# Performance work log

Hardware: AMD Instinct MI355X
Metric: run time of the kernel (lower is better)

Reference implementation:

```python
import jax, jax.numpy as jnp
import numpy as np

B, N, FEAT, MSG, LINK_H, CLS = 8, 128, 1024, 256, 512, 600
PROP = 2  # propagate_layers


def setup_inputs() -> dict:
    key = jax.random.key(0)
    ks = jax.random.split(key, 16)
    g = lambda k, shape, s=0.02: jax.random.normal(k, shape, dtype=jnp.float32) * s
    inp = {
        'edge_features': g(ks[0], (B, N, N, FEAT), 1.0),
        'node_features': g(ks[1], (B, N, FEAT), 1.0),
        'adj_mat': jnp.zeros((B, N, N), jnp.float32),          # shape placeholder only
        'node_labels': jnp.zeros((B, N, CLS), jnp.float32),    # shape placeholder only
        'human_nums': 64,
        'obj_nums': 64,
        # feature resize linears (Linear(FEAT -> MSG))
        'W_er': g(ks[2], (MSG, FEAT)), 'b_er': jnp.zeros((MSG,), jnp.float32),
        'W_nr': g(ks[3], (MSG, FEAT)), 'b_nr': jnp.zeros((MSG,), jnp.float32),
        # link fun (GraphConv): 1x1 Conv2d(MSG->LINK_H), ReLU, 1x1 Conv2d(LINK_H->1)
        'W_l1': g(ks[4], (LINK_H, MSG)), 'b_l1': jnp.zeros((LINK_H,), jnp.float32),
        'W_l2': g(ks[5], (1, LINK_H)), 'b_l2': jnp.zeros((1,), jnp.float32),
        # message fun linear_concat_relu: Linear(node+edge = 2*MSG -> MSG), ReLU
        'W_m': g(ks[6], (MSG, 2 * MSG)), 'b_m': jnp.zeros((MSG,), jnp.float32),
        # GRU(input=MSG, hidden=MSG), single layer single step
        'W_ih': g(ks[7], (3 * MSG, MSG)), 'b_ih': jnp.zeros((3 * MSG,), jnp.float32),
        'W_hh': g(ks[8], (3 * MSG, MSG)), 'b_hh': jnp.zeros((3 * MSG,), jnp.float32),
        # readout fc: Linear(MSG -> CLS)
        'W_r': g(ks[9], (CLS, MSG)), 'b_r': jnp.zeros((CLS,), jnp.float32),
    }
    return inp


def reference(edge_features, node_features, adj_mat, node_labels,
              human_nums, obj_nums,
              W_er, b_er, W_nr, b_nr, W_l1, b_l1, W_l2, b_l2,
              W_m, b_m, W_ih, b_ih, W_hh, b_hh, W_r, b_r):
    # valid_node_num = human_nums + obj_nums == N for every batch element.
    # Resize raw features to message size.
    e = edge_features @ W_er.T + b_er        # [B, v, w, MSG]
    h = node_features @ W_nr.T + b_nr        # [B, w, MSG]  (node states are never rewritten in source)
    # Split concat-linear into two matmuls to avoid materializing [B,N,N,2*MSG].
    W_mh, W_me = W_m[:, :MSG], W_m[:, MSG:]
    msg_h = jnp.einsum('bwd,md->bwm', h, W_mh)                 # node part, shared over target v
    msg_e = jnp.einsum('bvwd,md->bvwm', e, W_me) + b_m          # edge part (original e, constant over rounds)
    edge_state = e
    m = None
    pred_adj = None
    for _ in range(PROP):
        # link fun: per-(v,w) MLP over channels (1x1 convs)
        x = jax.nn.relu(edge_state @ W_l1.T + b_l1)             # [B,v,w,LINK_H]
        pred_adj = (x @ W_l2.T + b_l2)[..., 0]                  # [B,N,N]
        sig = jax.nn.sigmoid(pred_adj)
        # message fun linear_concat_relu, gated by predicted adjacency
        m = jax.nn.relu(msg_h[:, None, :, :] + msg_e)           # [B,v,w,MSG]
        m = sig[..., None] * m
        # hidden_edge_states[round+1][:, :, w, v] = m_v[:, :, w]
        edge_state = jnp.swapaxes(m, 1, 2)
    # node update happens per node each round but hidden node states are never
    # written back in the source, so only the last round's GRU step matters.
    m_sum = m.sum(axis=2)                                       # [B,v,MSG]
    gi = m_sum @ W_ih.T + b_ih
    gh = h @ W_hh.T + b_hh
    ir, iz, inn = jnp.split(gi, 3, axis=-1)
    hr, hz, hn = jnp.split(gh, 3, axis=-1)
    r = jax.nn.sigmoid(ir + hr)
    z = jax.nn.sigmoid(iz + hz)
    n = jnp.tanh(inn + r * hn)
    h_new = (1.0 - z) * n + z * h                               # [B,N,MSG]
    pred_node_labels = h_new @ W_r.T + b_r                      # [B,N,CLS]
    return pred_adj, pred_node_labels
```

## Files before the change

### kernel.cpp

```cpp
#include <hip/hip_runtime.h>
#include <cstdint>
#include <cstddef>

#define NND   128
#define FEATD 1024
#define MSGD  256
#define LHD   512
#define CLSD  600
#define LDST  264

typedef __bf16 bf16_t;
typedef bf16_t bf16x8 __attribute__((ext_vector_type(8)));
typedef float  f32x4  __attribute__((ext_vector_type(4)));
typedef unsigned short u16;
typedef u16 u16x8 __attribute__((ext_vector_type(8)));
typedef u16 u16x4 __attribute__((ext_vector_type(4)));

static __device__ __forceinline__ float bf2f(u16 u) {
  union { unsigned u; float f; } x; x.u = ((unsigned)u) << 16; return x.f;
}
static __device__ __forceinline__ u16 f2bf(float f) {
  union { float f; unsigned u; } x; x.f = f;
  return (u16)((x.u + 0x7fffu + ((x.u >> 16) & 1u)) >> 16);
}
static __device__ __forceinline__ f32x4 mfma16(u16x8 a, u16x8 b, f32x4 c) {
  return __builtin_amdgcn_mfma_f32_16x16x32_bf16(
      __builtin_bit_cast(bf16x8, a), __builtin_bit_cast(bf16x8, b), c, 0, 0, 0);
}
static __device__ __forceinline__ f32x4 zero4() {
  f32x4 v; v[0] = 0.f; v[1] = 0.f; v[2] = 0.f; v[3] = 0.f; return v;
}
static __device__ __forceinline__ float sigm(float x) { return 1.0f / (1.0f + expf(-x)); }

__global__ void k_cvt(const float* __restrict__ src, u16* __restrict__ dst, int n) {
  int i = (blockIdx.x * 256 + threadIdx.x) * 4;
  if (i + 3 < n) {
    float4 f = *(const float4*)(src + i);
    u16x4 o; o[0] = f2bf(f.x); o[1] = f2bf(f.y); o[2] = f2bf(f.z); o[3] = f2bf(f.w);
    *(u16x4*)(dst + i) = o;
  }
}

__global__ __launch_bounds__(256) void k_comb(const float* __restrict__ Wm,
                                              const float* __restrict__ Wer,
                                              const float* __restrict__ b_er,
                                              const float* __restrict__ b_m,
                                              u16* __restrict__ WcombB,
                                              float* __restrict__ bcomb) {
  const int m = blockIdx.x >> 2, ch = blockIdx.x & 3;
  const int d = ch * 256 + threadIdx.x;
  float s = 0.f;
  for (int k = 0; k < 256; ++k)
    s += Wm[(size_t)m * 512 + 256 + k] * Wer[(size_t)k * FEATD + d];
  WcombB[(size_t)m * FEATD + d] = f2bf(s);
  if (ch == 0 && threadIdx.x == 0) {
    float bb2 = b_m[m];
    for (int k = 0; k < 256; ++k) bb2 += Wm[(size_t)m * 512 + 256 + k] * b_er[k];
    bcomb[m] = bb2;
  }
}

__global__ __launch_bounds__(256) void s1_hmsg(const float* __restrict__ node,
                                               const float* __restrict__ Wnr,
                                               const float* __restrict__ bnr,
                                               const float* __restrict__ Wm,
                                               float* __restrict__ h32,
                                               u16* __restrict__ msghB) {
  __shared__ float nrow[FEATD];
  __shared__ float hrow[MSGD];
  const int r = blockIdx.x;
  const int t = threadIdx.x;
  *(float4*)(&nrow[t * 4]) = *(const float4*)(node + (size_t)r * FEATD + t * 4);
  __syncthreads();
  float acc = bnr[t];
  for (int d = 0; d < FEATD; ++d) acc += nrow[d] * Wnr[(size_t)t * FEATD + d];
  h32[(size_t)r * MSGD + t] = acc;
  hrow[t] = acc;
  __syncthreads();
  float mh = 0.f;
  for (int k = 0; k < MSGD; ++k) mh += hrow[k] * Wm[(size_t)t * 2 * MSGD + k];
  msghB[(size_t)r * MSGD + t] = f2bf(mh);
}

__global__ __launch_bounds__(512, 4) void k_main(
    const float* __restrict__ edge, const u16* __restrict__ Wer, const u16* __restrict__ Wm,
    const u16* __restrict__ Wl1, const float* __restrict__ b_er, const float* __restrict__ b_m,
    const float* __restrict__ b_l1, const float* __restrict__ W_l2, const float* __restrict__ b_l2,
    const u16* __restrict__ msgh, u16* __restrict__ M0g, float* __restrict__ pa_out) {
  __shared__ __align__(16) u16 lsE[64][LDST];
  __shared__ __align__(16) u16 lsM[64][LDST];
  __shared__ float lsPA[8][64];
  __shared__ float lsSig[64];

  const int tid = threadIdx.x, lane = tid & 63, wave = tid >> 6;
  const int lh = lane & 15, lq = lane >> 4;
  const int base = blockIdx.x * 64;
  const int bb = base >> 14;
  const int vv = (base >> 7) & 127;
  const int w0 = base & 127;

  f32x4 acc[4][4];

#pragma unroll
  for (int m = 0; m < 4; ++m)
#pragma unroll
    for (int t = 0; t < 2; ++t) acc[m][t] = zero4();
  for (int kc = 0; kc < 4; ++kc) {
#pragma unroll
    for (int i = 0; i < 8; ++i) {
      int idx = tid + i * 512;
      int row = idx >> 6;
      int c4 = (idx & 63) << 2;
      float4 f = *(const float4*)(edge + (size_t)(base + row) * FEATD + kc * 256 + c4);
      u16x4 o; o[0] = f2bf(f.x); o[1] = f2bf(f.y); o[2] = f2bf(f.z); o[3] = f2bf(f.w);
      *(u16x4*)(&lsE[row][c4]) = o;
    }
    __syncthreads();
#pragma unroll
    for (int ks = 0; ks < 8; ++ks) {
      u16x8 afr[4];
#pragma unroll
      for (int m = 0; m < 4; ++m) afr[m] = *(const u16x8*)(&lsE[16 * m + lh][ks * 32 + lq * 8]);
      const int kg = kc * 256 + ks * 32 + lq * 8;
#pragma unroll
      for (int t = 0; t < 2; ++t) {
        int col = wave * 32 + t * 16 + lh;
        u16x8 bfr = *(const u16x8*)(Wer + (size_t)col * FEATD + kg);
#pragma unroll
        for (int m = 0; m < 4; ++m) acc[m][t] = mfma16(afr[m], bfr, acc[m][t]);
      }
    }
    __syncthreads();
  }
#pragma unroll
  for (int t = 0; t < 2; ++t) {
    int col = wave * 32 + t * 16 + lh;
    float be = b_er[col];
#pragma unroll
    for (int m = 0; m < 4; ++m)
#pragma unroll
      for (int j = 0; j < 4; ++j)
        lsE[16 * m + 4 * lq + j][col] = f2bf(acc[m][t][j] + be);
  }
  __syncthreads();

  float prow[4][4];
#pragma unroll
  for (int m = 0; m < 4; ++m)
#pragma unroll
    for (int j = 0; j < 4; ++j) prow[m][j] = 0.f;
#pragma unroll
  for (int m = 0; m < 4; ++m)
#pragma unroll
    for (int t = 0; t < 4; ++t) acc[m][t] = zero4();
#pragma unroll
  for (int ks = 0; ks < 8; ++ks) {
    u16x8 afr[4];
#pragma unroll
    for (int m = 0; m < 4; ++m) afr[m] = *(const u16x8*)(&lsE[16 * m + lh][ks * 32 + lq * 8]);
    const int kg = ks * 32 + lq * 8;
#pragma unroll
    for (int t = 0; t < 4; ++t) {
      int col = wave * 64 + t * 16 + lh;
      u16x8 bfr = *(const u16x8*)(Wl1 + (size_t)col * MSGD + kg);
#pragma unroll
      for (int m = 0; m < 4; ++m) acc[m][t] = mfma16(afr[m], bfr, acc[m][t]);
    }
  }
#pragma unroll
  for (int t = 0; t < 4; ++t) {
    int col = wave * 64 + t * 16 + lh;
    float bl = b_l1[col], wl = W_l2[col];
#pragma unroll
    for (int m = 0; m < 4; ++m)
#pragma unroll
      for (int j = 0; j < 4; ++j) prow[m][j] += fmaxf(acc[m][t][j] + bl, 0.f) * wl;
  }
#pragma unroll
  for (int off = 1; off < 16; off <<= 1)
#pragma unroll
    for (int m = 0; m < 4; ++m)
#pragma unroll
      for (int j = 0; j < 4; ++j) prow[m][j] += __shfl_xor(prow[m][j], off, 64);
  if (lh == 0) {
#pragma unroll
    for (int m = 0; m < 4; ++m)
#pragma unroll
      for (int j = 0; j < 4; ++j) lsPA[wave][16 * m + 4 * lq + j] = prow[m][j];
  }
  __syncthreads();
  if (tid < 64) {
    float pa1 = b_l2[0];
#pragma unroll
    for (int g = 0; g < 8; ++g) pa1 += lsPA[g][tid];
    lsSig[tid] = sigm(pa1);
  }
#pragma unroll
  for (int i = 0; i < 4; ++i) {
    int idx = tid + i * 512;
    int row = idx >> 5;
    int c8 = (idx & 31) << 3;
    *(u16x8*)(&lsM[row][c8]) =
        *(const u16x8*)(msgh + (size_t)(bb * NND + w0 + row) * MSGD + c8);
  }
  __syncthreads();

#pragma unroll
  for (int m = 0; m < 4; ++m)
#pragma unroll
    for (int t = 0; t < 2; ++t) acc[m][t] = zero4();
#pragma unroll
  for (int ks = 0; ks < 8; ++ks) {
    u16x8 afr[4];
#pragma unroll
    for (int m = 0; m < 4; ++m) afr[m] = *(const u16x8*)(&lsE[16 * m + lh][ks * 32 + lq * 8]);
    const int kg = ks * 32 + lq * 8;
#pragma unroll
    for (int t = 0; t < 2; ++t) {
      int col = wave * 32 + t * 16 + lh;
      u16x8 bfr = *(const u16x8*)(Wm + (size_t)col * 512 + 256 + kg);
#pragma unroll
      for (int m = 0; m < 4; ++m) acc[m][t] = mfma16(afr[m], bfr, acc[m][t]);
    }
  }
#pragma unroll
  for (int t = 0; t < 2; ++t) {
    int col = wave * 32 + t * 16 + lh;
    float bm = b_m[col];
#pragma unroll
    for (int m = 0; m < 4; ++m)
#pragma unroll
      for (int j = 0; j < 4; ++j) {
        int row = 16 * m + 4 * lq + j;
        float mh = bf2f(lsM[row][col]);
        float m0 = fmaxf(acc[m][t][j] + bm + mh, 0.f);
        lsM[row][col] = f2bf(m0);
      }
  }
  __syncthreads();
#pragma unroll
  for (int i = 0; i < 4; ++i) {
    int idx = tid + i * 512;
    int row = idx >> 5;
    int c8 = (idx & 31) << 3;
    u16x8 m0v = *(const u16x8*)(&lsM[row][c8]);
    if (M0g) *(u16x8*)(M0g + (size_t)(base + row) * MSGD + c8) = m0v;
    float s = lsSig[row];
    u16x8 sc;
#pragma unroll
    for (int j = 0; j < 8; ++j) sc[j] = f2bf(bf2f(m0v[j]) * s);
    *(u16x8*)(&lsM[row][c8]) = sc;
  }
  __syncthreads();

#pragma unroll
  for (int m = 0; m < 4; ++m)
#pragma unroll
    for (int j = 0; j < 4; ++j) prow[m][j] = 0.f;
#pragma unroll
  for (int m = 0; m < 4; ++m)
#pragma unroll
    for (int t = 0; t < 4; ++t) acc[m][t] = zero4();
#pragma unroll
  for (int ks = 0; ks < 8; ++ks) {
    u16x8 afr[4];
#pragma unroll
    for (int m = 0; m < 4; ++m) afr[m] = *(const u16x8*)(&lsM[16 * m + lh][ks * 32 + lq * 8]);
    const int kg = ks * 32 + lq * 8;
#pragma unroll
    for (int t = 0; t < 4; ++t) {
      int col = wave * 64 + t * 16 + lh;
      u16x8 bfr = *(const u16x8*)(Wl1 + (size_t)col * MSGD + kg);
#pragma unroll
      for (int m = 0; m < 4; ++m) acc[m][t] = mfma16(afr[m], bfr, acc[m][t]);
    }
  }
#pragma unroll
  for (int t = 0; t < 4; ++t) {
    int col = wave * 64 + t * 16 + lh;
    float bl = b_l1[col], wl = W_l2[col];
#pragma unroll
    for (int m = 0; m < 4; ++m)
#pragma unroll
      for (int j = 0; j < 4; ++j) prow[m][j] += fmaxf(acc[m][t][j] + bl, 0.f) * wl;
  }
#pragma unroll
  for (int off = 1; off < 16; off <<= 1)
#pragma unroll
    for (int m = 0; m < 4; ++m)
#pragma unroll
      for (int j = 0; j < 4; ++j) prow[m][j] += __shfl_xor(prow[m][j], off, 64);
  if (lh == 0) {
#pragma unroll
    for (int m = 0; m < 4; ++m)
#pragma unroll
      for (int j = 0; j < 4; ++j) lsPA[wave][16 * m + 4 * lq + j] = prow[m][j];
  }
  __syncthreads();
  if (tid < 64) {
    float q = b_l2[0];
#pragma unroll
    for (int g = 0; g < 8; ++g) q += lsPA[g][tid];
    size_t o = ((size_t)bb * NND + (w0 + tid)) * NND + vv;
    pa_out[o] = q;
  }
}

__global__ __launch_bounds__(256) void k_msum_lite(const u16* __restrict__ M0g,
                                                   const float* __restrict__ qv,
                                                   float* __restrict__ msum) {
  __shared__ float sig[128];
  const int bv = blockIdx.x, tid = threadIdx.x;
  if (tid < 128) sig[tid] = sigm(qv[(size_t)bv * NND + tid]);
  __syncthreads();
  const u16* p = M0g + (size_t)bv * NND * MSGD + tid;
  float a = 0.f;
#pragma unroll 8
  for (int w = 0; w < 128; ++w) a += sig[w] * bf2f(p[(size_t)w * MSGD]);
  msum[(size_t)bv * MSGD + tid] = a;
}

__global__ __launch_bounds__(256, 2) void k_msum2(
    const float* __restrict__ edge, const u16* __restrict__ Wcomb,
    const float* __restrict__ bcomb, const u16* __restrict__ msgh,
    const float* __restrict__ qv, float* __restrict__ msum) {
  __shared__ __align__(16) u16 lsE[64][LDST];
  __shared__ __align__(16) u16 lsM[64][LDST];
  __shared__ float lsSig[64];
  const int tid = threadIdx.x, lane = tid & 63, wave = tid >> 6;
  const int lh = lane & 15, lq = lane >> 4;
  const int bv = blockIdx.x;
  const int bb = bv >> 7;

  float csum[4] = {0.f, 0.f, 0.f, 0.f};

  for (int hh = 0; hh < 2; ++hh) {
    if (tid < 64) lsSig[tid] = sigm(qv[(size_t)bv * NND + hh * 64 + tid]);
#pragma unroll
    for (int i = 0; i < 8; ++i) {
      int idx = tid + i * 256;
      int row = idx >> 5;
      int c8 = (idx & 31) << 3;
      *(u16x8*)(&lsM[row][c8]) =
          *(const u16x8*)(msgh + (size_t)(bb * NND + hh * 64 + row) * MSGD + c8);
    }
    f32x4 acc[4][4];
#pragma unroll
    for (int m = 0; m < 4; ++m)
#pragma unroll
      for (int t = 0; t < 4; ++t) acc[m][t] = zero4();

    for (int kc = 0; kc < 4; ++kc) {
#pragma unroll
      for (int i = 0; i < 16; ++i) {
        int idx = tid + i * 256;
        int row = idx >> 6;
        int c4 = (idx & 63) << 2;
        float4 f = *(const float4*)(edge + (size_t)(bv * NND + hh * 64 + row) * FEATD + kc * 256 + c4);
        u16x4 o; o[0] = f2bf(f.x); o[1] = f2bf(f.y); o[2] = f2bf(f.z); o[3] = f2bf(f.w);
        *(u16x4*)(&lsE[row][c4]) = o;
      }
      __syncthreads();
#pragma unroll
      for (int ks = 0; ks < 8; ++ks) {
        u16x8 afr[4];
#pragma unroll
        for (int m = 0; m < 4; ++m) afr[m] = *(const u16x8*)(&lsE[16 * m + lh][ks * 32 + lq * 8]);
        const int kg = kc * 256 + ks * 32 + lq * 8;
#pragma unroll
        for (int t = 0; t < 4; ++t) {
          int col = wave * 64 + t * 16 + lh;
          u16x8 bfr = *(const u16x8*)(Wcomb + (size_t)col * FEATD + kg);
#pragma unroll
          for (int m = 0; m < 4; ++m) acc[m][t] = mfma16(afr[m], bfr, acc[m][t]);
        }
      }
      __syncthreads();
    }
#pragma unroll
    for (int t = 0; t < 4; ++t) {
      int col = wave * 64 + t * 16 + lh;
      float bc = bcomb[col];
#pragma unroll
      for (int m = 0; m < 4; ++m)
#pragma unroll
        for (int j = 0; j < 4; ++j) {
          int row = 16 * m + 4 * lq + j;
          float m0 = fmaxf(acc[m][t][j] + bc + bf2f(lsM[row][col]), 0.f);
          csum[t] += lsSig[row] * m0;
        }
    }
    __syncthreads();
  }
#pragma unroll
  for (int off = 16; off < 64; off <<= 1)
#pragma unroll
    for (int t = 0; t < 4; ++t) csum[t] += __shfl_xor(csum[t], off, 64);
  if (lq == 0) {
#pragma unroll
    for (int t = 0; t < 4; ++t)
      msum[(size_t)bv * MSGD + wave * 64 + t * 16 + lh] = csum[t];
  }
}

__global__ __launch_bounds__(256) void k_gru(const float* __restrict__ msum,
                                             const float* __restrict__ h32,
                                             const float* __restrict__ Wih, const float* __restrict__ bih,
                                             const float* __restrict__ Whh, const float* __restrict__ bhh,
                                             const float* __restrict__ Wr, const float* __restrict__ br,
                                             float* __restrict__ outlab) {
  __shared__ __align__(16) float sM[8][256];
  __shared__ __align__(16) float sH[8][256];
  __shared__ __align__(16) float sHn[8][256];
  const int tid = threadIdx.x;
  const int r0 = blockIdx.x * 8;
#pragma unroll
  for (int i = 0; i < 2; ++i) {
    int idx = tid + i * 256;
    int row = idx >> 6;
    int c = (idx & 63) << 2;
    *(float4*)(&sM[row][c]) = *(const float4*)(msum + (size_t)(r0 + row) * 256 + c);
    *(float4*)(&sH[row][c]) = *(const float4*)(h32 + (size_t)(r0 + row) * 256 + c);
  }
  __syncthreads();
  float gi[3][8], gh[3][8];
#pragma unroll
  for (int c = 0; c < 3; ++c) {
    float bi_ = bih[tid + 256 * c], bh_ = bhh[tid + 256 * c];
#pragma unroll
    for (int rr = 0; rr < 8; ++rr) { gi[c][rr] = bi_; gh[c][rr] = bh_; }
  }
  for (int k = 0; k < 256; k += 4) {
    float4 wi[3], wh[3];
#pragma unroll
    for (int c = 0; c < 3; ++c) {
      wi[c] = *(const float4*)(Wih + (size_t)(tid + 256 * c) * 256 + k);
      wh[c] = *(const float4*)(Whh + (size_t)(tid + 256 * c) * 256 + k);
    }
#pragma unroll
    for (int rr = 0; rr < 8; ++rr) {
      float4 ms = *(const float4*)(&sM[rr][k]);
      float4 hh = *(const float4*)(&sH[rr][k]);
#pragma unroll
      for (int c = 0; c < 3; ++c) {
        gi[c][rr] += wi[c].x * ms.x + wi[c].y * ms.y + wi[c].z * ms.z + wi[c].w * ms.w;
        gh[c][rr] += wh[c].x * hh.x + wh[c].y * hh.y + wh[c].z * hh.z + wh[c].w * hh.w;
      }
    }
  }
#pragma unroll
  for (int rr = 0; rr < 8; ++rr) {
    float r = sigm(gi[0][rr] + gh[0][rr]);
    float z = sigm(gi[1][rr] + gh[1][rr]);
    float n = tanhf(gi[2][rr] + r * gh[2][rr]);
    sHn[rr][tid] = (1.f - z) * n + z * sH[rr][tid];
  }
  __syncthreads();
  float lab[3][8];
  int cs[3]; bool has[3];
#pragma unroll
  for (int c = 0; c < 3; ++c) {
    cs[c] = tid + 256 * c;
    has[c] = cs[c] < CLSD;
    float b0 = has[c] ? br[cs[c]] : 0.f;
#pragma unroll
    for (int rr = 0; rr < 8; ++rr) lab[c][rr] = b0;
  }
  for (int k = 0; k < 256; k += 4) {
    float4 wr[3];
#pragma unroll
    for (int c = 0; c < 3; ++c) {
      if (has[c]) wr[c] = *(const float4*)(Wr + (size_t)cs[c] * 256 + k);
      else { wr[c].x = 0.f; wr[c].y = 0.f; wr[c].z = 0.f; wr[c].w = 0.f; }
    }
#pragma unroll
    for (int rr = 0; rr < 8; ++rr) {
      float4 hv = *(const float4*)(&sHn[rr][k]);
#pragma unroll
      for (int c = 0; c < 3; ++c)
        lab[c][rr] += wr[c].x * hv.x + wr[c].y * hv.y + wr[c].z * hv.z + wr[c].w * hv.w;
    }
  }
#pragma unroll
  for (int c = 0; c < 3; ++c) {
    if (has[c]) {
#pragma unroll
      for (int rr = 0; rr < 8; ++rr)
        outlab[(size_t)(r0 + rr) * CLSD + cs[c]] = lab[c][rr];
    }
  }
}

extern "C" void kernel_launch(void* const* d_in, const int* in_sizes, int n_in,
                              void* d_out, int out_size, void* d_ws, size_t ws_size,
                              hipStream_t stream) {
  const float* edge = (const float*)d_in[0];
  const float* node = (const float*)d_in[1];
  const float* W_er = (const float*)d_in[6];
  const float* b_er = (const float*)d_in[7];
  const float* W_nr = (const float*)d_in[8];
  const float* b_nr = (const float*)d_in[9];
  const float* W_l1 = (const float*)d_in[10];
  const float* b_l1 = (const float*)d_in[11];
  const float* W_l2 = (const float*)d_in[12];
  const float* b_l2 = (const float*)d_in[13];
  const float* W_m  = (const float*)d_in[14];
  const float* b_m  = (const float*)d_in[15];
  const float* W_ih = (const float*)d_in[16];
  const float* b_ih = (const float*)d_in[17];
  const float* W_hh = (const float*)d_in[18];
  const float* b_hh = (const float*)d_in[19];
  const float* W_r  = (const float*)d_in[20];
  const float* b_r  = (const float*)d_in[21];

  char* ws = (char*)d_ws;
  size_t off = 0;
  auto alloc = [&](size_t bytes) -> void* {
    void* p = ws + off;
    off += (bytes + 511) & ~(size_t)511;
    return p;
  };
  u16* WerB     = (u16*)alloc((size_t)262144 * 2);
  u16* WmB      = (u16*)alloc((size_t)131072 * 2);
  u16* Wl1B     = (u16*)alloc((size_t)131072 * 2);
  u16* WcombB   = (u16*)alloc((size_t)262144 * 2);
  float* bcombF = (float*)alloc((size_t)256 * 4);
  u16* msghB    = (u16*)alloc((size_t)262144 * 2);
  float* h32    = (float*)alloc((size_t)262144 * 4);
  float* msum   = (float*)alloc((size_t)262144 * 4);
  u16* M0g      = (u16*)alloc((size_t)33554432 * 2);
  const bool fast = (ws_size >= off);
  u16* M0arg = fast ? M0g : (u16*)nullptr;

  float* out_pa  = (float*)d_out;
  float* out_lab = out_pa + 131072;

  k_cvt  <<<256,  256, 0, stream>>>(W_er, WerB, 262144);
  k_cvt  <<<128,  256, 0, stream>>>(W_m,  WmB,  131072);
  k_cvt  <<<128,  256, 0, stream>>>(W_l1, Wl1B, 131072);
  if (!fast)
    k_comb<<<1024, 256, 0, stream>>>(W_m, W_er, b_er, b_m, WcombB, bcombF);
  s1_hmsg<<<1024, 256, 0, stream>>>(node, W_nr, b_nr, W_m, h32, msghB);
  k_main <<<2048, 512, 0, stream>>>(edge, WerB, WmB, Wl1B, b_er, b_m, b_l1, W_l2, b_l2,
                                    msghB, M0arg, out_pa);
  if (fast)
    k_msum_lite<<<1024, 256, 0, stream>>>(M0g, out_pa, msum);
  else
    k_msum2<<<1024, 256, 0, stream>>>(edge, WcombB, bcombF, msghB, out_pa, msum);
  k_gru  <<<128,  256, 0, stream>>>(msum, h32, W_ih, b_ih, W_hh, b_hh, W_r, b_r, out_lab);
}
```

Measured before the change: 729.9 us.

## Pre-convert edge features to bf16 and stage via async global-to-LDS loads

New measurement: 915.4 us. +25.4%, slower.

```diff
diff --git a/kernel.cpp b/kernel.cpp
--- a/kernel.cpp
+++ b/kernel.cpp
@@ -32,12 +32,31 @@
 }
 static __device__ __forceinline__ float sigm(float x) { return 1.0f / (1.0f + expf(-x)); }
 
+#define GLD16(gsrc, ldst)                                                      \
+  __builtin_amdgcn_global_load_lds(                                            \
+      (const __attribute__((address_space(1))) unsigned int*)(gsrc),           \
+      (__attribute__((address_space(3))) unsigned int*)(ldst), 16, 0, 0)
+
 __global__ void k_cvt(const float* __restrict__ src, u16* __restrict__ dst, int n) {
   int i = (blockIdx.x * 256 + threadIdx.x) * 4;
   if (i + 3 < n) {
     float4 f = *(const float4*)(src + i);
     u16x4 o; o[0] = f2bf(f.x); o[1] = f2bf(f.y); o[2] = f2bf(f.z); o[3] = f2bf(f.w);
     *(u16x4*)(dst + i) = o;
+  }
+}
+
+__global__ __launch_bounds__(256) void k_cvt_edge(const float* __restrict__ src,
+                                                  u16* __restrict__ dst, long n) {
+  long i = ((long)blockIdx.x * 256 + threadIdx.x) * 8;
+  const long stride = (long)gridDim.x * 256 * 8;
+  for (; i + 7 < n; i += stride) {
+    float4 a = *(const float4*)(src + i);
+    float4 b = *(const float4*)(src + i + 4);
+    u16x8 o;
+    o[0] = f2bf(a.x); o[1] = f2bf(a.y); o[2] = f2bf(a.z); o[3] = f2bf(a.w);
+    o[4] = f2bf(b.x); o[5] = f2bf(b.y); o[6] = f2bf(b.z); o[7] = f2bf(b.w);
+    *(u16x8*)(dst + i) = o;
   }
 }
 
@@ -82,7 +101,233 @@
   msghB[(size_t)r * MSGD + t] = f2bf(mh);
 }
 
-__global__ __launch_bounds__(512, 4) void k_main(
+__global__ __launch_bounds__(512, 4) void k_main_bf(
+    const u16* __restrict__ edgeB, const u16* __restrict__ Wer, const u16* __restrict__ Wm,
+    const u16* __restrict__ Wl1, const float* __restrict__ b_er, const float* __restrict__ b_m,
+    const float* __restrict__ b_l1, const float* __restrict__ W_l2, const float* __restrict__ b_l2,
+    const u16* __restrict__ msgh, u16* __restrict__ M0g, float* __restrict__ pa_out) {
+  __shared__ __align__(16) u16 lsS0[64 * 256];
+  __shared__ __align__(16) u16 lsS1[64 * 256];
+  __shared__ float lsPA[8][64];
+  __shared__ float lsSig[64];
+
+  const int tid = threadIdx.x, lane = tid & 63, wave = tid >> 6;
+  const int lh = lane & 15, lq = lane >> 4;
+  const int base = blockIdx.x * 64;
+  const int bb = base >> 14, vv = (base >> 7) & 127, w0 = base & 127;
+
+  auto ELP = [&](u16* b, int row, int bo) -> u16* {
+    return (u16*)((char*)b + row * 512 + (bo ^ ((row & 7) << 4)));
+  };
+  auto STAGE = [&](int kc, int pb) {
+    char* bufc = (char*)(pb ? lsS1 : lsS0);
+#pragma unroll
+    for (int i = 0; i < 4; ++i) {
+      int r = i * 16 + (tid >> 5);
+      int sb = (((tid & 31) * 16) ^ (((tid >> 5) & 7) << 4));
+      const char* gsrc = (const char*)edgeB + ((size_t)(base + r) * 2048) + kc * 512 + sb;
+      char* ldst = bufc + i * 8192 + wave * 1024;
+      GLD16(gsrc, ldst);
+    }
+  };
+
+  f32x4 acc[4][4];
+
+#pragma unroll
+  for (int m = 0; m < 4; ++m)
+#pragma unroll
+    for (int t = 0; t < 2; ++t) acc[m][t] = zero4();
+  STAGE(0, 0);
+  __syncthreads();
+  for (int kc = 0; kc < 4; ++kc) {
+    if (kc < 3) STAGE(kc + 1, (kc + 1) & 1);
+    u16* sb = (kc & 1) ? lsS1 : lsS0;
+    const int kg0 = kc * 256;
+#pragma unroll
+    for (int ks = 0; ks < 8; ++ks) {
+      u16x8 afr[4];
+#pragma unroll
+      for (int m = 0; m < 4; ++m)
+        afr[m] = *(const u16x8*)ELP(sb, 16 * m + lh, ks * 64 + lq * 16);
+      const int kg = kg0 + ks * 32 + lq * 8;
+#pragma unroll
+      for (int t = 0; t < 2; ++t) {
+        int col = wave * 32 + t * 16 + lh;
+        u16x8 bfr = *(const u16x8*)(Wer + (size_t)col * FEATD + kg);
+#pragma unroll
+        for (int m = 0; m < 4; ++m) acc[m][t] = mfma16(afr[m], bfr, acc[m][t]);
+      }
+    }
+    __syncthreads();
+  }
+#pragma unroll
+  for (int t = 0; t < 2; ++t) {
+    int col = wave * 32 + t * 16 + lh;
+    float be = b_er[col];
+#pragma unroll
+    for (int m = 0; m < 4; ++m)
+#pragma unroll
+      for (int j = 0; j < 4; ++j)
+        *ELP(lsS0, 16 * m + 4 * lq + j, col * 2) = f2bf(acc[m][t][j] + be);
+  }
+  __syncthreads();
+
+  float prow[4][4];
+#pragma unroll
+  for (int m = 0; m < 4; ++m)
+#pragma unroll
+    for (int j = 0; j < 4; ++j) prow[m][j] = 0.f;
+#pragma unroll
+  for (int m = 0; m < 4; ++m)
+#pragma unroll
+    for (int t = 0; t < 4; ++t) acc[m][t] = zero4();
+#pragma unroll
+  for (int ks = 0; ks < 8; ++ks) {
+    u16x8 afr[4];
+#pragma unroll
+    for (int m = 0; m < 4; ++m)
+      afr[m] = *(const u16x8*)ELP(lsS0, 16 * m + lh, ks * 64 + lq * 16);
+    const int kg = ks * 32 + lq * 8;
+#pragma unroll
+    for (int t = 0; t < 4; ++t) {
+      int col = wave * 64 + t * 16 + lh;
+      u16x8 bfr = *(const u16x8*)(Wl1 + (size_t)col * MSGD + kg);
+#pragma unroll
+      for (int m = 0; m < 4; ++m) acc[m][t] = mfma16(afr[m], bfr, acc[m][t]);
+    }
+  }
+#pragma unroll
+  for (int t = 0; t < 4; ++t) {
+    int col = wave * 64 + t * 16 + lh;
+    float bl = b_l1[col], wl = W_l2[col];
+#pragma unroll
+    for (int m = 0; m < 4; ++m)
+#pragma unroll
+      for (int j = 0; j < 4; ++j) prow[m][j] += fmaxf(acc[m][t][j] + bl, 0.f) * wl;
+  }
+#pragma unroll
+  for (int off = 1; off < 16; off <<= 1)
+#pragma unroll
+    for (int m = 0; m < 4; ++m)
+#pragma unroll
+      for (int j = 0; j < 4; ++j) prow[m][j] += __shfl_xor(prow[m][j], off, 64);
+  if (lh == 0) {
+#pragma unroll
+    for (int m = 0; m < 4; ++m)
+#pragma unroll
+      for (int j = 0; j < 4; ++j) lsPA[wave][16 * m + 4 * lq + j] = prow[m][j];
+  }
+  __syncthreads();
+  if (tid < 64) {
+    float pa1 = b_l2[0];
+#pragma unroll
+    for (int g = 0; g < 8; ++g) pa1 += lsPA[g][tid];
+    lsSig[tid] = sigm(pa1);
+  }
+
+#pragma unroll
+  for (int m = 0; m < 4; ++m)
+#pragma unroll
+    for (int t = 0; t < 2; ++t) acc[m][t] = zero4();
+#pragma unroll
+  for (int ks = 0; ks < 8; ++ks) {
+    u16x8 afr[4];
+#pragma unroll
+    for (int m = 0; m < 4; ++m)
+      afr[m] = *(const u16x8*)ELP(lsS0, 16 * m + lh, ks * 64 + lq * 16);
+    const int kg = ks * 32 + lq * 8;
+#pragma unroll
+    for (int t = 0; t < 2; ++t) {
+      int col = wave * 32 + t * 16 + lh;
+      u16x8 bfr = *(const u16x8*)(Wm + (size_t)col * 512 + 256 + kg);
+#pragma unroll
+      for (int m = 0; m < 4; ++m) acc[m][t] = mfma16(afr[m], bfr, acc[m][t]);
+    }
+  }
+#pragma unroll
+  for (int t = 0; t < 2; ++t) {
+    int col = wave * 32 + t * 16 + lh;
+    float bm = b_m[col];
+#pragma unroll
+    for (int m = 0; m < 4; ++m)
+#pragma unroll
+      for (int j = 0; j < 4; ++j) {
+        int row = 16 * m + 4 * lq + j;
+        float mh = bf2f(msgh[(size_t)(bb * NND + w0 + row) * MSGD + col]);
+        *ELP(lsS1, row, col * 2) = f2bf(fmaxf(acc[m][t][j] + bm + mh, 0.f));
+      }
+  }
+  __syncthreads();
+#pragma unroll
+  for (int i = 0; i < 4; ++i) {
+    int idx = tid + i * 512;
+    int row = idx >> 5;
+    int c8 = (idx & 31) << 3;
+    u16x8 m0v = *(const u16x8*)ELP(lsS1, row, c8 * 2);
+    if (M0g) *(u16x8*)(M0g + (size_t)(base + row) * MSGD + c8) = m0v;
+    float s = lsSig[row];
+    u16x8 sc;
+#pragma unroll
+    for (int j = 0; j < 8; ++j) sc[j] = f2bf(bf2f(m0v[j]) * s);
+    *(u16x8*)ELP(lsS1, row, c8 * 2) = sc;
+  }
+  __syncthreads();
+
+#pragma unroll
+  for (int m = 0; m < 4; ++m)
+#pragma unroll
+    for (int j = 0; j < 4; ++j) prow[m][j] = 0.f;
+#pragma unroll
+  for (int m = 0; m < 4; ++m)
+#pragma unroll
+    for (int t = 0; t < 4; ++t) acc[m][t] = zero4();
+#pragma unroll
+  for (int ks = 0; ks < 8; ++ks) {
+    u16x8 afr[4];
+#pragma unroll
+    for (int m = 0; m < 4; ++m)
+      afr[m] = *(const u16x8*)ELP(lsS1, 16 * m + lh, ks * 64 + lq * 16);
+    const int kg = ks * 32 + lq * 8;
+#pragma unroll
+    for (int t = 0; t < 4; ++t) {
+      int col = wave * 64 + t * 16 + lh;
+      u16x8 bfr = *(const u16x8*)(Wl1 + (size_t)col * MSGD + kg);
+#pragma unroll
+      for (int m = 0; m < 4; ++m) acc[m][t] = mfma16(afr[m], bfr, acc[m][t]);
+    }
+  }
+#pragma unroll
+  for (int t = 0; t < 4; ++t) {
+    int col = wave * 64 + t * 16 + lh;
+    float bl = b_l1[col], wl = W_l2[col];
+#pragma unroll
+    for (int m = 0; m < 4; ++m)
+#pragma unroll
+      for (int j = 0; j < 4; ++j) prow[m][j] += fmaxf(acc[m][t][j] + bl, 0.f) * wl;
+  }
+#pragma unroll
+  for (int off = 1; off < 16; off <<= 1)
+#pragma unroll
+    for (int m = 0; m < 4; ++m)
+#pragma unroll
+      for (int j = 0; j < 4; ++j) prow[m][j] += __shfl_xor(prow[m][j], off, 64);
+  if (lh == 0) {
+#pragma unroll
+    for (int m = 0; m < 4; ++m)
+#pragma unroll
+      for (int j = 0; j < 4; ++j) lsPA[wave][16 * m + 4 * lq + j] = prow[m][j];
+  }
+  __syncthreads();
+  if (tid < 64) {
+    float q = b_l2[0];
+#pragma unroll
+    for (int g = 0; g < 8; ++g) q += lsPA[g][tid];
+    size_t o = ((size_t)bb * NND + (w0 + tid)) * NND + vv;
+    pa_out[o] = q;
+  }
+}
+
+__global__ __launch_bounds__(512, 4) void k_main_f32(
     const float* __restrict__ edge, const u16* __restrict__ Wer, const u16* __restrict__ Wm,
     const u16* __restrict__ Wl1, const float* __restrict__ b_er, const float* __restrict__ b_m,
     const float* __restrict__ b_l1, const float* __restrict__ W_l2, const float* __restrict__ b_l2,
@@ -233,8 +478,7 @@
       for (int j = 0; j < 4; ++j) {
         int row = 16 * m + 4 * lq + j;
         float mh = bf2f(lsM[row][col]);
-        float m0 = fmaxf(acc[m][t][j] + bm + mh, 0.f);
-        lsM[row][col] = f2bf(m0);
+        lsM[row][col] = f2bf(fmaxf(acc[m][t][j] + bm + mh, 0.f));
       }
   }
   __syncthreads();
@@ -529,8 +773,10 @@
   float* h32    = (float*)alloc((size_t)262144 * 4);
   float* msum   = (float*)alloc((size_t)262144 * 4);
   u16* M0g      = (u16*)alloc((size_t)33554432 * 2);
-  const bool fast = (ws_size >= off);
-  u16* M0arg = fast ? M0g : (u16*)nullptr;
+  size_t off_m0 = off;
+  u16* edgeB    = (u16*)alloc((size_t)134217728 * 2);
+  size_t off_eb = off;
+  const int tier = (ws_size >= off_eb) ? 0 : (ws_size >= off_m0 ? 1 : 2);
 
   float* out_pa  = (float*)d_out;
   float* out_lab = out_pa + 131072;
@@ -538,14 +784,22 @@
   k_cvt  <<<256,  256, 0, stream>>>(W_er, WerB, 262144);
   k_cvt  <<<128,  256, 0, stream>>>(W_m,  WmB,  131072);
   k_cvt  <<<128,  256, 0, stream>>>(W_l1, Wl1B, 131072);
-  if (!fast)
+  s1_hmsg<<<1024, 256, 0, stream>>>(node, W_nr, b_nr, W_m, h32, msghB);
+
+  if (tier == 0) {
+    k_cvt_edge<<<2048, 256, 0, stream>>>(edge, edgeB, (long)134217728);
+    k_main_bf <<<2048, 512, 0, stream>>>(edgeB, WerB, WmB, Wl1B, b_er, b_m, b_l1, W_l2, b_l2,
+                                         msghB, M0g, out_pa);
+    k_msum_lite<<<1024, 256, 0, stream>>>(M0g, out_pa, msum);
+  } else if (tier == 1) {
+    k_main_f32<<<2048, 512, 0, stream>>>(edge, WerB, WmB, Wl1B, b_er, b_m, b_l1, W_l2, b_l2,
+                                         msghB, M0g, out_pa);
+    k_msum_lite<<<1024, 256, 0, stream>>>(M0g, out_pa, msum);
+  } else {
     k_comb<<<1024, 256, 0, stream>>>(W_m, W_er, b_er, b_m, WcombB, bcombF);
-  s1_hmsg<<<1024, 256, 0, stream>>>(node, W_nr, b_nr, W_m, h32, msghB);
-  k_main <<<2048, 512, 0, stream>>>(edge, WerB, WmB, Wl1B, b_er, b_m, b_l1, W_l2, b_l2,
-                                    msghB, M0arg, out_pa);
-  if (fast)
-    k_msum_lite<<<1024, 256, 0, stream>>>(M0g, out_pa, msum);
-  else
+    k_main_f32<<<2048, 512, 0, stream>>>(edge, WerB, WmB, Wl1B, b_er, b_m, b_l1, W_l2, b_l2,
+                                         msghB, (u16*)nullptr, out_pa);
     k_msum2<<<1024, 256, 0, stream>>>(edge, WcombB, bcombF, msghB, out_pa, msum);
-  k_gru  <<<128,  256, 0, stream>>>(msum, h32, W_ih, b_ih, W_hh, b_hh, W_r, b_r, out_lab);
-}
+  }
+  k_gru<<<128, 256, 0, stream>>>(msum, h32, W_ih, b_ih, W_hh, b_hh, W_r, b_r, out_lab);
+}
```
